# Performance work log

Measured on AMD Instinct MI355X. Metric: run time of the kernel, lower is better.

Reference implementation:

```python
import jax, jax.numpy as jnp
import numpy as np

LAYER_SIZES = [1024, 1024, 1024, 1024, 1024, 1024, 512]
MAX_PATHS = 128
BATCH = 128
N_LAYERS = len(LAYER_SIZES) - 1


def setup_inputs() -> dict:
    key = jax.random.key(0)
    keys = jax.random.split(key, 1 + 2 * N_LAYERS)
    inp = {"x": jax.random.normal(keys[0], (BATCH, LAYER_SIZES[0]), dtype=jnp.float32)}
    for i in range(N_LAYERS):
        inp[f"W{i}"] = jax.random.normal(keys[1 + 2 * i], (LAYER_SIZES[i], LAYER_SIZES[i + 1]), dtype=jnp.float32) * 0.01
        inp[f"b{i}"] = jax.random.normal(keys[2 + 2 * i], (LAYER_SIZES[i + 1],), dtype=jnp.float32) * 0.01
    return inp


def _layer(data, W, b):
    # data: [B, in_feat, P] -> [B, out_feat, 3P]
    B, _, P = data.shape
    O = W.shape[1]
    pos = jnp.einsum('bfp,fo->bpo', data, W) + b          # [B, P, O]; neg branch is exactly -pos
    branches = jnp.stack([-pos, jnp.zeros_like(pos), pos], axis=-1)  # [B, P, O, 3]
    # transpose(1,2) then reshape: interleave branches per source path, matching torch
    return branches.transpose(0, 2, 1, 3).reshape(B, O, P * 3)


def _prune(data, keep):
    # keep top-`keep` paths by L2 norm over the feature dim
    norms = jnp.linalg.norm(data, axis=1)                 # [B, P]
    _, idx = jax.lax.top_k(norms, keep)                   # [B, keep]
    return jnp.take_along_axis(data, idx[:, None, :], axis=-1)


def _forward(x, Ws, bs):
    data = x[:, :, None]                                   # [B, F, 1]
    for i in range(N_LAYERS):
        data = _layer(data, Ws[i], bs[i])
        if i < N_LAYERS - 1:
            data = jnp.tanh(data)
        if data.shape[-1] > MAX_PATHS:
            data = _prune(data, MAX_PATHS)
    # collapse with 'max_abs': per (batch, feature) pick path with largest |value|
    idx = jnp.argmax(jnp.abs(data), axis=-1, keepdims=True)
    output = jnp.take_along_axis(data, idx, axis=-1).squeeze(-1)
    return output, data


def reference(x, W0, b0, W1, b1, W2, b2, W3, b3, W4, b4, W5, b5):
    Ws = [W0, W1, W2, W3, W4, W5]
    bs = [b0, b1, b2, b3, b4, b5]
    return _forward(x, Ws, bs)
```

## Files before the change

kernel.cpp:

```cpp
#include <hip/hip_runtime.h>
#include <math.h>


using s8v = __attribute__((ext_vector_type(8))) short;
using f4v = __attribute__((ext_vector_type(4))) float;

__device__ __forceinline__ float bf2f(short b) {
  unsigned u = ((unsigned)(unsigned short)b) << 16;
  return __builtin_bit_cast(float, u);
}
__device__ __forceinline__ short f2bf(float f) {
  unsigned u = __builtin_bit_cast(unsigned, f);
  u = (u + 0x7FFFu + ((u >> 16) & 1u)) >> 16;
  return (short)u;
}
__device__ __forceinline__ void split_store(float f, short* hi, short* lo) {
  short h = f2bf(f);
  *hi = h;
  *lo = f2bf(f - bf2f(h));
}

struct TWArgs {
  const float* W[6];
  short* Th[6];
  short* Tl[6];
};
__global__ void __launch_bounds__(256)
transW_all(TWArgs a, const float* __restrict__ x, short* __restrict__ A0h,
           short* __restrict__ A0l, float4* __restrict__ zreg) {
  __shared__ float tile[64][65];
  const int t = threadIdx.x;
  if (blockIdx.z == 6) {
    const int bf = blockIdx.y * 16 + blockIdx.x;
    if (bf < 128) {
      int i = (bf * 256 + t) * 4;
      float4 v = *(const float4*)&x[i];
      short4 h, l;
      h.x = f2bf(v.x); l.x = f2bf(v.x - bf2f(h.x));
      h.y = f2bf(v.y); l.y = f2bf(v.y - bf2f(h.y));
      h.z = f2bf(v.z); l.z = f2bf(v.z - bf2f(h.z));
      h.w = f2bf(v.w); l.w = f2bf(v.w - bf2f(h.w));
      *(short4*)&A0h[i] = h;
      *(short4*)&A0l[i] = l;
    } else {
      int flat = (bf - 128) * 256 + t;
      if (flat < 1984) {
        float4 zz = {0.f, 0.f, 0.f, 0.f};
        zreg[flat] = zz;
      }
    }
    return;
  }
  const int z = blockIdx.z;
  const int N = (z == 5) ? 512 : 1024;
  const int n0 = blockIdx.x * 64, k0 = blockIdx.y * 64;
  if (n0 >= N) return;
  const float* __restrict__ W = a.W[z];
  short* __restrict__ Th = a.Th[z];
  short* __restrict__ Tl = a.Tl[z];
  const int r = t >> 4, c4 = (t & 15) * 4;
#pragma unroll
  for (int i = 0; i < 4; ++i) {
    int rr = r + 16 * i;
    float4 v = *(const float4*)&W[(size_t)(k0 + rr) * N + n0 + c4];
    tile[rr][c4 + 0] = v.x;
    tile[rr][c4 + 1] = v.y;
    tile[rr][c4 + 2] = v.z;
    tile[rr][c4 + 3] = v.w;
  }
  __syncthreads();
#pragma unroll
  for (int i = 0; i < 4; ++i) {
    int n = r + 16 * i;
    short4 h, l;
    float f0 = tile[c4 + 0][n], f1 = tile[c4 + 1][n];
    float f2 = tile[c4 + 2][n], f3 = tile[c4 + 3][n];
    h.x = f2bf(f0); l.x = f2bf(f0 - bf2f(h.x));
    h.y = f2bf(f1); l.y = f2bf(f1 - bf2f(h.y));
    h.z = f2bf(f2); l.z = f2bf(f2 - bf2f(h.z));
    h.w = f2bf(f3); l.w = f2bf(f3 - bf2f(h.w));
    size_t o = (size_t)(n0 + n) * 1024 + k0 + c4;
    *(short4*)&Th[o] = h;
    *(short4*)&Tl[o] = l;
  }
}

template <int MODE, int D, int KS>
__device__ __forceinline__ void gemm_body(
    int bx, int by, int bz, int R, const short* __restrict__ Ah,
    const short* __restrict__ Al, const short* __restrict__ Bh,
    const short* __restrict__ Bl, const float* __restrict__ bias,
    short* __restrict__ Oh, short* __restrict__ Ol, float* __restrict__ Of,
    float* __restrict__ aux0, float* __restrict__ aux1, int N, int Dn) {
  constexpr int KC = 1024 / KS;
  constexpr int BKP = 32;
  __shared__ short As_h[64 * BKP], As_l[64 * BKP];
  __shared__ short Bs_h[64 * BKP], Bs_l[64 * BKP];
  const int t = threadIdx.x;
  const int row0 = by * 64;
  const int col0 = bx * 64;
  const int kb = bz * KC;
  const int sr = t >> 2, sko = (t & 3) * 8;
  const short* Ahp = Ah + (size_t)(row0 + sr) * 1024 + kb + sko;
  const short* Alp = Al + (size_t)(row0 + sr) * 1024 + kb + sko;
  const short* Bhp = Bh + (size_t)(col0 + sr) * 1024 + kb + sko;
  const short* Blp = Bl + (size_t)(col0 + sr) * 1024 + kb + sko;
  const int wofs = (t >> 6) * 512;
  short* dAh = &As_h[wofs];
  short* dAl = &As_l[wofs];
  short* dBh = &Bs_h[wofs];
  short* dBl = &Bs_l[wofs];
  const int w = t >> 6, lane = t & 63;
  const int l16 = lane & 15, q = lane >> 4;
  const int wm0 = (w & 1) * 32, wn0 = (w >> 1) * 32;
  const int abase = (wm0 + l16) * BKP + q * 8;
  const int bbase = (wn0 + l16) * BKP + q * 8;
  f4v acc[2][2];
#pragma unroll
  for (int i = 0; i < 2; ++i)
#pragma unroll
    for (int j = 0; j < 2; ++j) acc[i][j] = (f4v){0.f, 0.f, 0.f, 0.f};
  for (int k0 = 0; k0 < KC; k0 += 32) {
    __syncthreads();
    __builtin_amdgcn_global_load_lds(Ahp + k0, dAh, 16, 0, 0);
    __builtin_amdgcn_global_load_lds(Alp + k0, dAl, 16, 0, 0);
    __builtin_amdgcn_global_load_lds(Bhp + k0, dBh, 16, 0, 0);
    __builtin_amdgcn_global_load_lds(Blp + k0, dBl, 16, 0, 0);
    __syncthreads();
    s8v ah[2], al[2], bh[2], bl[2];
#pragma unroll
    for (int mt = 0; mt < 2; ++mt) {
      ah[mt] = *(const s8v*)&As_h[abase + mt * 16 * BKP];
      al[mt] = *(const s8v*)&As_l[abase + mt * 16 * BKP];
    }
#pragma unroll
    for (int nt = 0; nt < 2; ++nt) {
      bh[nt] = *(const s8v*)&Bs_h[bbase + nt * 16 * BKP];
      bl[nt] = *(const s8v*)&Bs_l[bbase + nt * 16 * BKP];
    }
#pragma unroll
    for (int mt = 0; mt < 2; ++mt)
#pragma unroll
      for (int nt = 0; nt < 2; ++nt) {
        acc[mt][nt] = __builtin_amdgcn_mfma_f32_16x16x32_bf16(
            ah[mt], bh[nt], acc[mt][nt], 0, 0, 0);
        acc[mt][nt] = __builtin_amdgcn_mfma_f32_16x16x32_bf16(
            ah[mt], bl[nt], acc[mt][nt], 0, 0, 0);
        acc[mt][nt] = __builtin_amdgcn_mfma_f32_16x16x32_bf16(
            al[mt], bh[nt], acc[mt][nt], 0, 0, 0);
      }
  }

  if (MODE == 2) {
    const float bc0 = bias[col0 + wn0 + l16];
    const float bc1 = bias[col0 + wn0 + 16 + l16];
#pragma unroll
    for (int mt = 0; mt < 2; ++mt) {
#pragma unroll
      for (int r = 0; r < 4; ++r) {
        const int rr = row0 + wm0 + mt * 16 + q * 4 + r;
        float sd = 0.f, sn = 0.f;
#pragma unroll
        for (int nt = 0; nt < 2; ++nt) {
          const int gcol = col0 + wn0 + nt * 16 + l16;
          const float bc = nt ? bc1 : bc0;
          const float v = acc[mt][nt][r];
          Of[(size_t)rr * N + gcol] = v;
          sd = fmaf(bc, v, sd);
          sn = fmaf(v, v, sn);
        }
#pragma unroll
        for (int d = 1; d < 16; d <<= 1) {
          sd += __shfl_xor(sd, d);
          sn += __shfl_xor(sn, d);
        }
        if (l16 == 0) {
          atomicAdd(&aux0[rr], sd);
          atomicAdd(&aux1[rr], sn);
        }
      }
    }
    return;
  }

#pragma unroll
  for (int nt = 0; nt < 2; ++nt) {
    int gcol = col0 + wn0 + nt * 16 + l16;
    float bc = (MODE == 1) ? bias[gcol] : 0.f;
#pragma unroll
    for (int mt = 0; mt < 2; ++mt) {
#pragma unroll
      for (int r = 0; r < 4; ++r) {
        float v = acc[mt][nt][r];
        int rr = row0 + wm0 + mt * 16 + q * 4 + r;
        if (MODE == 1) {
          int b = rr / D, u = rr - b * D;
          size_t ob = (size_t)(b * Dn) * N + gcol;
          size_t om = ob + (size_t)(1 + 2 * u) * N;
          size_t op = ob + (size_t)(2 + 2 * u) * N;
          split_store(tanhf(bc - v), &Oh[om], &Ol[om]);
          split_store(tanhf(bc + v), &Oh[op], &Ol[op]);
          if (u == 0) split_store(tanhf(bc), &Oh[ob], &Ol[ob]);
        } else {
          Of[((size_t)bz * R + rr) * N + gcol] = v;
        }
      }
    }
  }
}

template <int MODE, int D, int KS>
__global__ void __launch_bounds__(256, 2)
mfma_gemm(const short* __restrict__ Ah, const short* __restrict__ Al,
          const short* __restrict__ Bh, const short* __restrict__ Bl,
          const float* __restrict__ bias, short* __restrict__ Oh,
          short* __restrict__ Ol, float* __restrict__ Of,
          float* __restrict__ aux0, float* __restrict__ aux1, int N, int Dn) {
  gemm_body<MODE, D, KS>(blockIdx.x, blockIdx.y, blockIdx.z,
                         (int)gridDim.y << 6, Ah, Al, Bh, Bl, bias, Oh, Ol,
                         Of, aux0, aux1, N, Dn);
}

__device__ __forceinline__ void rownorm_body(const short* __restrict__ hi,
                                             const short* __restrict__ lo,
                                             float* __restrict__ ns, int row) {
  int t = threadIdx.x;
  size_t base = (size_t)row * 1024 + t * 4;
  short4 h = *(const short4*)&hi[base];
  short4 l = *(const short4*)&lo[base];
  float v0 = bf2f(h.x) + bf2f(l.x);
  float v1 = bf2f(h.y) + bf2f(l.y);
  float v2 = bf2f(h.z) + bf2f(l.z);
  float v3 = bf2f(h.w) + bf2f(l.w);
  float s = v0 * v0 + v1 * v1 + v2 * v2 + v3 * v3;
  __shared__ float red[256];
  red[t] = s;
  __syncthreads();
  for (int off = 128; off; off >>= 1) {
    if (t < off) red[t] += red[t + off];
    __syncthreads();
  }
  if (t == 0) ns[row] = red[0];
}

__global__ void __launch_bounds__(256, 2)
gemm5_rownorm(const short* __restrict__ C5h, const short* __restrict__ C5l,
              const short* __restrict__ W5h, const short* __restrict__ W5l,
              const float* __restrict__ b5, float* __restrict__ Y5,
              float* __restrict__ ns, float* __restrict__ dotv,
              float* __restrict__ nrmv) {
  const int bid = blockIdx.x;
  if (bid < 496) {
    gemm_body<2, 31, 1>(bid & 7, bid >> 3, 0, 0, C5h, C5l, W5h, W5l, b5,
                        nullptr, nullptr, Y5, dotv, nrmv, 512, 0);
  } else {
    rownorm_body(C5h, C5l, ns, bid - 496);
  }
}

template <int KS>
__global__ void __launch_bounds__(256)
comb0_hl(const float* __restrict__ P, const float* __restrict__ bias,
         short* __restrict__ Oh, short* __restrict__ Ol, int R, int N) {
  int i = blockIdx.x * 256 + threadIdx.x;
  int n4 = N >> 2;
  int r = i / n4, c4 = (i - r * n4) * 4;
  float4 y = *(const float4*)&P[(size_t)r * N + c4];
  size_t stride = (size_t)R * N;
#pragma unroll
  for (int ks = 1; ks < KS; ++ks) {
    const float4 p = *(const float4*)&P[ks * stride + (size_t)r * N + c4];
    y.x += p.x; y.y += p.y; y.z += p.z; y.w += p.w;
  }
  float4 bc = *(const float4*)(bias + c4);
  float t0 = tanhf(bc.x + y.x), t1 = tanhf(bc.y + y.y);
  float t2 = tanhf(bc.z + y.z), t3 = tanhf(bc.w + y.w);
  short4 h, l;
  h.x = f2bf(t0); l.x = f2bf(t0 - bf2f(h.x));
  h.y = f2bf(t1); l.y = f2bf(t1 - bf2f(h.y));
  h.z = f2bf(t2); l.z = f2bf(t2 - bf2f(h.z));
  h.w = f2bf(t3); l.w = f2bf(t3 - bf2f(h.w));
  *(short4*)&Oh[(size_t)r * N + c4] = h;
  *(short4*)&Ol[(size_t)r * N + c4] = l;
}

template <int KS, int D>
__global__ void __launch_bounds__(256)
comb1_hl(const float* __restrict__ P, const float* __restrict__ bias,
         short* __restrict__ Oh, short* __restrict__ Ol, int R, int N,
         int Dn) {
  int i = blockIdx.x * 256 + threadIdx.x;
  int n4 = N >> 2;
  int r = i / n4, c4 = (i - r * n4) * 4;
  int b = r / D, u = r - b * D;
  float4 y = *(const float4*)&P[(size_t)r * N + c4];
  size_t stride = (size_t)R * N;
#pragma unroll
  for (int ks = 1; ks < KS; ++ks) {
    const float4 p = *(const float4*)&P[ks * stride + (size_t)r * N + c4];
    y.x += p.x; y.y += p.y; y.z += p.z; y.w += p.w;
  }
  float4 bc = *(const float4*)(bias + c4);
  size_t ob = (size_t)(b * Dn) * N + c4;
  size_t om = ob + (size_t)(1 + 2 * u) * N;
  size_t op = ob + (size_t)(2 + 2 * u) * N;
  {
    float t0 = tanhf(bc.x - y.x), t1 = tanhf(bc.y - y.y);
    float t2 = tanhf(bc.z - y.z), t3 = tanhf(bc.w - y.w);
    short4 h, l;
    h.x = f2bf(t0); l.x = f2bf(t0 - bf2f(h.x));
    h.y = f2bf(t1); l.y = f2bf(t1 - bf2f(h.y));
    h.z = f2bf(t2); l.z = f2bf(t2 - bf2f(h.z));
    h.w = f2bf(t3); l.w = f2bf(t3 - bf2f(h.w));
    *(short4*)&Oh[om] = h;
    *(short4*)&Ol[om] = l;
  }
  {
    float t0 = tanhf(bc.x + y.x), t1 = tanhf(bc.y + y.y);
    float t2 = tanhf(bc.z + y.z), t3 = tanhf(bc.w + y.w);
    short4 h, l;
    h.x = f2bf(t0); l.x = f2bf(t0 - bf2f(h.x));
    h.y = f2bf(t1); l.y = f2bf(t1 - bf2f(h.y));
    h.z = f2bf(t2); l.z = f2bf(t2 - bf2f(h.z));
    h.w = f2bf(t3); l.w = f2bf(t3 - bf2f(h.w));
    *(short4*)&Oh[op] = h;
    *(short4*)&Ol[op] = l;
  }
  if (u == 0) {
    float t0 = tanhf(bc.x), t1 = tanhf(bc.y);
    float t2 = tanhf(bc.z), t3 = tanhf(bc.w);
    short4 h, l;
    h.x = f2bf(t0); l.x = f2bf(t0 - bf2f(h.x));
    h.y = f2bf(t1); l.y = f2bf(t1 - bf2f(h.y));
    h.z = f2bf(t2); l.z = f2bf(t2 - bf2f(h.z));
    h.w = f2bf(t3); l.w = f2bf(t3 - bf2f(h.w));
    *(short4*)&Oh[ob] = h;
    *(short4*)&Ol[ob] = l;
  }
}

__global__ void __launch_bounds__(384)
prune45_k(const float* __restrict__ ns, const float* __restrict__ dotv,
          const float* __restrict__ nrmv, const float* __restrict__ b5,
          int* __restrict__ kept4, int* __restrict__ kept5) {
  const int b = blockIdx.x, t = threadIdx.x;
  __shared__ float nss[31];
  __shared__ float rb[256];
  __shared__ float keyA[243];
  __shared__ int cls[243];
  __shared__ int k4s[128];
  __shared__ float pns[128];
  __shared__ float keyB[384];
  if (t < 31) nss[t] = ns[b * 31 + t];
  if (t < 256) {
    float a = b5[t], c = b5[t + 256];
    rb[t] = fmaf(a, a, 0.f);
    rb[t] = fmaf(c, c, rb[t]);
  }
  __syncthreads();
  for (int off = 128; off; off >>= 1) {
    if (t < off) rb[t] += rb[t + off];
    __syncthreads();
  }
  const float nb5 = rb[0];
  if (t < 243) {
    int j = t / 3, t4 = t - 3 * j;
    int d0 = j / 27, d1 = (j / 9) % 3, d2 = (j / 3) % 3, d3 = j % 3;
    int u = 0;
    u = (d0 == 1) ? 0 : (1 + 2 * u + (d0 == 2));
    u = (d1 == 1) ? 0 : (1 + 2 * u + (d1 == 2));
    u = (d2 == 1) ? 0 : (1 + 2 * u + (d2 == 2));
    u = (d3 == 1) ? 0 : (1 + 2 * u + (d3 == 2));
    cls[t] = u;
    keyA[t] = (t4 == 1) ? 0.f : nss[u];
  }
  __syncthreads();
  if (t < 243) {
    float k = keyA[t];
    int rank = 0;
    for (int e = 0; e < 243; ++e) {
      float ke = keyA[e];
      rank += (ke > k) || (ke == k && e < t);
    }
    if (rank < 128) {
      int t4 = t - 3 * (t / 3);
      int kv = (cls[t] << 1) | (t4 == 2 ? 1 : 0);
      k4s[rank] = kv;
      kept4[b * 128 + rank] = kv;
    }
  }
  __syncthreads();
  if (t < 128) {
    int k4 = k4s[t];
    int c = k4 >> 1;
    float s = (k4 & 1) ? 1.f : -1.f;
    pns[t] = nb5 + nrmv[b * 31 + c] + s * 2.f * dotv[b * 31 + c];
  }
  __syncthreads();
  const int m = t / 3, tt = t - 3 * m;
  keyB[t] = (tt == 1) ? 0.f : pns[m];
  __syncthreads();
  float k = keyB[t];
  int rank = 0;
  for (int e = 0; e < 384; ++e) {
    float ke = keyB[e];
    rank += (ke > k) || (ke == k && e < t);
  }
  if (rank < 128) kept5[b * 128 + rank] = (m << 1) | (tt == 2 ? 1 : 0);
}

__global__ void __launch_bounds__(256)
finalize_k(const float* __restrict__ Y5, const float* __restrict__ b5,
           const int* __restrict__ kept4, const int* __restrict__ kept5,
           float* __restrict__ out, float* __restrict__ dataout) {
  const int b = blockIdx.y;
  const int o0 = blockIdx.x * 64;
  __shared__ float Ys[31][65];
  __shared__ float bias_s[64];
  __shared__ float vt[64][130];
  __shared__ float ra[64][4];
  __shared__ float rv[64][4];
  const int t = threadIdx.x;
  for (int idx = t; idx < 31 * 64; idx += 256) {
    int c = idx >> 6, o = idx & 63;
    Ys[c][o] = Y5[((size_t)b * 31 + c) * 512 + o0 + o];
  }
  if (t < 64) bias_s[t] = b5[o0 + t];
  const int rr = t & 127, oh = t >> 7;
  int k5 = kept5[b * 128 + rr];
  int m = k5 >> 1;
  float sig = (k5 & 1) ? 1.f : -1.f;
  int k4 = kept4[b * 128 + m];
  int cc = k4 >> 1;
  float s4 = (k4 & 1) ? 1.f : -1.f;
  float afac = sig * s4;
  __syncthreads();
#pragma unroll
  for (int ol = 0; ol < 32; ++ol) {
    int o = oh * 32 + ol;
    float v = sig * bias_s[o] + afac * Ys[cc][o];
    dataout[((size_t)b * 512 + o0 + o) * 128 + rr] = v;
    vt[o][rr] = v;
  }
  __syncthreads();
  int o = t >> 2, q = t & 3;
  float bestv = vt[o][q * 32];
  float besta = fabsf(bestv);
  for (int i = 1; i < 32; ++i) {
    float v = vt[o][q * 32 + i];
    float a = fabsf(v);
    if (a > besta) {
      besta = a;
      bestv = v;
    }
  }
  ra[o][q] = besta;
  rv[o][q] = bestv;
  __syncthreads();
  if (t < 64) {
    float ba = ra[t][0], bv = rv[t][0];
#pragma unroll
    for (int qq = 1; qq < 4; ++qq) {
      if (ra[t][qq] > ba) {
        ba = ra[t][qq];
        bv = rv[t][qq];
      }
    }
    out[(size_t)b * 512 + o0 + t] = bv;
  }
}

extern "C" void kernel_launch(void* const* d_in, const int* in_sizes, int n_in,
                              void* d_out, int out_size, void* d_ws,
                              size_t ws_size, hipStream_t stream) {
  const float* x = (const float*)d_in[0];
  const float* Wt[6];
  const float* bs[6];
  for (int i = 0; i < 6; ++i) {
    Wt[i] = (const float*)d_in[1 + 2 * i];
    bs[i] = (const float*)d_in[2 + 2 * i];
  }
  char* base = (char*)d_ws;
  short* A0h = (short*)(base + 0);
  short* A0l = (short*)(base + 262144);
  short* Wh[6], *Wl[6];
  {
    size_t off = 524288;
    for (int i = 0; i < 6; ++i) {
      size_t sz = (i < 5) ? 2097152 : 1048576;
      Wh[i] = (short*)(base + off);
      Wl[i] = (short*)(base + off + sz);
      off += 2 * sz;
    }
  }
  short* C1h = (short*)(base + 23592960), *C1l = (short*)(base + 23855104);
  short* C2h = (short*)(base + 24117248), *C2l = (short*)(base + 24903680);
  short* C3h = (short*)(base + 25690112), *C3l = (short*)(base + 27525120);
  short* C4h = (short*)(base + 29360128), *C4l = (short*)(base + 33292288);
  short* C5h = (short*)(base + 524288);
  short* C5l = (short*)(base + 8912896);
  float* PA = (float*)(base + 29360128);
  float* PB = (float*)(base + 524288);
  float* Y5 = (float*)(base + 23592960);
  char* zb = base + 37224448;
  float* dotv = (float*)zb;
  float* nrmv = (float*)(zb + 15872);
  float* ns = (float*)(zb + 31744);
  int* kept4 = (int*)(zb + 47616);
  int* kept5 = (int*)(zb + 113152);
  float* outp = (float*)d_out;
  float* dataout = outp + 128 * 512;

  dim3 blk(256);
  TWArgs twa;
  for (int i = 0; i < 6; ++i) {
    twa.W[i] = Wt[i];
    twa.Th[i] = Wh[i];
    twa.Tl[i] = Wl[i];
  }
  transW_all<<<dim3(16, 16, 7), blk, 0, stream>>>(twa, x, A0h, A0l,
                                                  (float4*)zb);
  mfma_gemm<3, 1, 8><<<dim3(16, 2, 8), blk, 0, stream>>>(
      A0h, A0l, Wh[0], Wl[0], nullptr, nullptr, nullptr, PA, nullptr, nullptr,
      1024, 0);
  comb0_hl<8><<<dim3(128), blk, 0, stream>>>(PA, bs[0], C1h, C1l, 128, 1024);
  mfma_gemm<3, 1, 8><<<dim3(16, 2, 8), blk, 0, stream>>>(
      C1h, C1l, Wh[1], Wl[1], nullptr, nullptr, nullptr, PA, nullptr, nullptr,
      1024, 0);
  comb1_hl<8, 1><<<dim3(128), blk, 0, stream>>>(PA, bs[1], C2h, C2l, 128, 1024,
                                                3);
  mfma_gemm<3, 3, 4><<<dim3(16, 6, 4), blk, 0, stream>>>(
      C2h, C2l, Wh[2], Wl[2], nullptr, nullptr, nullptr, PA, nullptr, nullptr,
      1024, 0);
  comb1_hl<4, 3><<<dim3(384), blk, 0, stream>>>(PA, bs[2], C3h, C3l, 384, 1024,
                                                7);
  mfma_gemm<3, 7, 2><<<dim3(16, 14, 2), blk, 0, stream>>>(
      C3h, C3l, Wh[3], Wl[3], nullptr, nullptr, nullptr, PB, nullptr, nullptr,
      1024, 0);
  comb1_hl<2, 7><<<dim3(896), blk, 0, stream>>>(PB, bs[3], C4h, C4l, 896, 1024,
                                                15);
  mfma_gemm<1, 15, 1><<<dim3(16, 30), blk, 0, stream>>>(
      C4h, C4l, Wh[4], Wl[4], bs[4], C5h, C5l, nullptr, nullptr, nullptr, 1024,
      31);
  gemm5_rownorm<<<dim3(496 + 3968), blk, 0, stream>>>(
      C5h, C5l, Wh[5], Wl[5], bs[5], Y5, ns, dotv, nrmv);
  prune45_k<<<dim3(128), dim3(384), 0, stream>>>(ns, dotv, nrmv, bs[5], kept4,
                                                 kept5);
  finalize_k<<<dim3(8, 128), blk, 0, stream>>>(Y5, bs[5], kept4, kept5, outp,
                                               dataout);
}
```

Before: 235.1 us.

## Double-buffer LDS tiles to overlap next global load with MFMA compute

```diff
diff --git a/kernel.cpp b/kernel.cpp
--- a/kernel.cpp
+++ b/kernel.cpp
@@ -94,8 +94,8 @@
     float* __restrict__ aux0, float* __restrict__ aux1, int N, int Dn) {
   constexpr int KC = 1024 / KS;
   constexpr int BKP = 32;
-  __shared__ short As_h[64 * BKP], As_l[64 * BKP];
-  __shared__ short Bs_h[64 * BKP], Bs_l[64 * BKP];
+  __shared__ short As_h[2][64 * BKP], As_l[2][64 * BKP];
+  __shared__ short Bs_h[2][64 * BKP], Bs_l[2][64 * BKP];
   const int t = threadIdx.x;
   const int row0 = by * 64;
   const int col0 = bx * 64;
@@ -106,10 +106,6 @@
   const short* Bhp = Bh + (size_t)(col0 + sr) * 1024 + kb + sko;
   const short* Blp = Bl + (size_t)(col0 + sr) * 1024 + kb + sko;
   const int wofs = (t >> 6) * 512;
-  short* dAh = &As_h[wofs];
-  short* dAl = &As_l[wofs];
-  short* dBh = &Bs_h[wofs];
-  short* dBl = &Bs_l[wofs];
   const int w = t >> 6, lane = t & 63;
   const int l16 = lane & 15, q = lane >> 4;
   const int wm0 = (w & 1) * 32, wn0 = (w >> 1) * 32;
@@ -120,23 +116,34 @@
   for (int i = 0; i < 2; ++i)
 #pragma unroll
     for (int j = 0; j < 2; ++j) acc[i][j] = (f4v){0.f, 0.f, 0.f, 0.f};
+  __builtin_amdgcn_global_load_lds(Ahp, &As_h[0][wofs], 16, 0, 0);
+  __builtin_amdgcn_global_load_lds(Alp, &As_l[0][wofs], 16, 0, 0);
+  __builtin_amdgcn_global_load_lds(Bhp, &Bs_h[0][wofs], 16, 0, 0);
+  __builtin_amdgcn_global_load_lds(Blp, &Bs_l[0][wofs], 16, 0, 0);
   for (int k0 = 0; k0 < KC; k0 += 32) {
+    const int cur = (k0 >> 5) & 1;
     __syncthreads();
-    __builtin_amdgcn_global_load_lds(Ahp + k0, dAh, 16, 0, 0);
-    __builtin_amdgcn_global_load_lds(Alp + k0, dAl, 16, 0, 0);
-    __builtin_amdgcn_global_load_lds(Bhp + k0, dBh, 16, 0, 0);
-    __builtin_amdgcn_global_load_lds(Blp + k0, dBl, 16, 0, 0);
-    __syncthreads();
+    if (k0 + 32 < KC) {
+      const int nxt = cur ^ 1;
+      __builtin_amdgcn_global_load_lds(Ahp + k0 + 32, &As_h[nxt][wofs], 16, 0,
+                                       0);
+      __builtin_amdgcn_global_load_lds(Alp + k0 + 32, &As_l[nxt][wofs], 16, 0,
+                                       0);
+      __builtin_amdgcn_global_load_lds(Bhp + k0 + 32, &Bs_h[nxt][wofs], 16, 0,
+                                       0);
+      __builtin_amdgcn_global_load_lds(Blp + k0 + 32, &Bs_l[nxt][wofs], 16, 0,
+                                       0);
+    }
     s8v ah[2], al[2], bh[2], bl[2];
 #pragma unroll
     for (int mt = 0; mt < 2; ++mt) {
-      ah[mt] = *(const s8v*)&As_h[abase + mt * 16 * BKP];
-      al[mt] = *(const s8v*)&As_l[abase + mt * 16 * BKP];
+      ah[mt] = *(const s8v*)&As_h[cur][abase + mt * 16 * BKP];
+      al[mt] = *(const s8v*)&As_l[cur][abase + mt * 16 * BKP];
     }
 #pragma unroll
     for (int nt = 0; nt < 2; ++nt) {
-      bh[nt] = *(const s8v*)&Bs_h[bbase + nt * 16 * BKP];
-      bl[nt] = *(const s8v*)&Bs_l[bbase + nt * 16 * BKP];
+      bh[nt] = *(const s8v*)&Bs_h[cur][bbase + nt * 16 * BKP];
+      bl[nt] = *(const s8v*)&Bs_l[cur][bbase + nt * 16 * BKP];
     }
 #pragma unroll
     for (int mt = 0; mt < 2; ++mt)
```

After: 248.4 us. +5.7%, slower.
